# Optimization experiments

Hardware: AMD Instinct MI355X
Metric: run time of the kernel (lower is better)

Reference implementation:

```python
import jax, jax.numpy as jnp
import numpy as np

KEEP_RATIO = 0.25
BLOCK = 8
TEMP = 0.1


def setup_inputs() -> dict:
    key = jax.random.key(0)
    features = jax.random.normal(key, (8, 256, 132, 132), dtype=jnp.float32)
    return {"features": features, "enabled": 1}


def reference(features, enabled):
    B, C, H, W = features.shape
    if not enabled:
        return jnp.ones((B, C, H, W), dtype=features.dtype)
    # pad H, W up to multiples of BLOCK (zeros, like F.pad default)
    ph = (-H) % BLOCK
    pw = (-W) % BLOCK
    x = jnp.pad(jnp.abs(features), ((0, 0), (0, 0), (0, ph), (0, pw)))
    Hp, Wp = H + ph, W + pw
    nh, nw = Hp // BLOCK, Wp // BLOCK
    # avg_pool2d(kernel=stride=BLOCK) == block-mean via reshape
    pooled = x.reshape(B, C, nh, BLOCK, nw, BLOCK).mean(axis=(3, 5))  # [B,C,nh,nw]
    total = nh * nw
    scores = pooled.reshape(B, C, total)
    keep = max(1, min(total, int(round(total * KEEP_RATIO))))
    top_vals, top_idx = jax.lax.top_k(scores, keep)  # sorted descending, like torch.topk
    # hard mask: scatter ones at topk indices
    flat_idx = top_idx.reshape(B * C, keep)
    hard = (jnp.zeros((B * C, total), dtype=features.dtype)
            .at[jnp.arange(B * C)[:, None], flat_idx].set(1.0)
            .reshape(B, C, total))
    # training-mode straight-through soft blend
    thr = jax.lax.stop_gradient(top_vals[..., -1:])  # kth value as threshold
    soft = jax.nn.sigmoid((scores - thr) / TEMP)
    soft = soft * (keep / jnp.maximum(soft.sum(-1, keepdims=True), 1e-6))
    soft = jnp.clip(soft, 0.0, 1.0)
    mask = jax.lax.stop_gradient(hard) - jax.lax.stop_gradient(soft) + soft
    # upsample blocks back to pixels (repeat_interleave) and crop padding
    block_mask = mask.reshape(B, C, nh, nw)
    full = jnp.repeat(jnp.repeat(block_mask, BLOCK, axis=2), BLOCK, axis=3)
    return full[:, :, :H, :W]
```

## Files before the change

### kernel.cpp

```cpp
#include <hip/hip_runtime.h>


#define HH 132
#define WW 132
#define NB 17
#define TOTAL 289
#define NKPAD 292
#define KEEP 72
#define NTH 256
#define NC4 33
#define NV 4356
#define PLANES 2048

typedef float floatx4 __attribute__((ext_vector_type(4)));

__global__ __launch_bounds__(NTH)
void gate_kernel(const float4* __restrict__ feats4,
                 const int* __restrict__ enabled_p,
                 float4* __restrict__ out4) {
    const int plane = blockIdx.x;
    const int t = threadIdx.x;
    const float4* __restrict__ fp = feats4 + (size_t)plane * NV;

    __shared__ __align__(16) float    s_e[NV];
    __shared__ __align__(16) unsigned s_key[NKPAD];
    __shared__ float s_hard[TOTAL];

    #pragma unroll
    for (int k = 0; k < 18; ++k) {
        const int v = t + k * NTH;
        if (v < NV) {
            const float4 x = fp[v];
            s_e[v] = (fabsf(x.x) + fabsf(x.y)) + (fabsf(x.z) + fabsf(x.w));
        }
    }
    __syncthreads();

    for (int b = t; b < TOTAL; b += NTH) {
        const int br = b / NB;
        const int bc = b - br * NB;
        const int nr = (br == NB - 1) ? 4 : 8;
        const int base = (br * 8) * NC4 + 2 * bc;
        double sum = 0.0;
        if (bc < NB - 1) {
            for (int rr = 0; rr < nr; ++rr)
                sum += (double)s_e[base + rr * NC4]
                     + (double)s_e[base + rr * NC4 + 1];
        } else {
            for (int rr = 0; rr < nr; ++rr)
                sum += (double)s_e[base + rr * NC4];
        }
        s_key[b] = __float_as_uint((float)sum);
    }
    if (t < NKPAD - TOTAL) s_key[TOTAL + t] = 0u;
    __syncthreads();

    const int en = *enabled_p;
    for (int i = t; i < TOTAL; i += NTH) {
        const unsigned ki = s_key[i];
        const int thr0 = (i + 3) >> 2;
        const int thr1 = (i + 2) >> 2;
        const int thr2 = (i + 1) >> 2;
        const int thr3 =  i      >> 2;
        const uint4* __restrict__ sk4 = (const uint4*)s_key;
        int rank = 0;
        #pragma unroll 8
        for (int q = 0; q < NKPAD / 4; ++q) {
            const uint4 k = sk4[q];
            rank += (int)((k.x > ki) || ((k.x == ki) && (q < thr0)));
            rank += (int)((k.y > ki) || ((k.y == ki) && (q < thr1)));
            rank += (int)((k.z > ki) || ((k.z == ki) && (q < thr2)));
            rank += (int)((k.w > ki) || ((k.w == ki) && (q < thr3)));
        }
        s_hard[i] = (!en || rank < KEEP) ? 1.0f : 0.0f;
    }
    __syncthreads();

    floatx4* __restrict__ op = (floatx4*)(out4 + (size_t)plane * NV);
    for (int v = t; v < NV; v += NTH) {
        const int base = v * 4;
        const int row = base / WW;
        const int col = base - row * WW;
        const float m = s_hard[(row >> 3) * NB + (col >> 3)];
        const floatx4 mv = {m, m, m, m};
        __builtin_nontemporal_store(mv, &op[v]);
    }
}

extern "C" void kernel_launch(void* const* d_in, const int* in_sizes, int n_in,
                              void* d_out, int out_size, void* d_ws, size_t ws_size,
                              hipStream_t stream) {
    const float4* feats = (const float4*)d_in[0];
    const int* enabled = (const int*)d_in[1];
    float4* out = (float4*)d_out;
    gate_kernel<<<PLANES, NTH, 0, stream>>>(feats, enabled, out);
}
```

Measured before the change: 256.2 us.

## Replace O(n^2) rank counting with wavefront radix-select threshold for top-k

Instead of each thread counting how many of the 289 keys exceed its own, a single wavefront does a 32-step bitwise radix select using ballot and popcount. This finds the k-th largest key and how many of the tied keys to keep. Each element then compares against that threshold, and only exact ties scan earlier indices so the lowest-index tie-break is preserved. It removes the quadratic LDS scan but adds an extra barrier and a serial phase run by only one wavefront.

Result: no change. 260.8 us (+1.8%).

```diff
diff --git a/kernel.cpp b/kernel.cpp
--- a/kernel.cpp
+++ b/kernel.cpp
@@ -5,7 +5,7 @@
 #define WW 132
 #define NB 17
 #define TOTAL 289
-#define NKPAD 292
+#define NPAD 320
 #define KEEP 72
 #define NTH 256
 #define NC4 33
@@ -23,8 +23,10 @@
     const float4* __restrict__ fp = feats4 + (size_t)plane * NV;
 
     __shared__ __align__(16) float    s_e[NV];
-    __shared__ __align__(16) unsigned s_key[NKPAD];
+    __shared__ __align__(16) unsigned s_key[NPAD];
     __shared__ float s_hard[TOTAL];
+    __shared__ unsigned s_T;
+    __shared__ int s_kT;
 
     #pragma unroll
     for (int k = 0; k < 18; ++k) {
@@ -36,43 +38,67 @@
     }
     __syncthreads();
 
-    for (int b = t; b < TOTAL; b += NTH) {
-        const int br = b / NB;
-        const int bc = b - br * NB;
-        const int nr = (br == NB - 1) ? 4 : 8;
-        const int base = (br * 8) * NC4 + 2 * bc;
-        double sum = 0.0;
-        if (bc < NB - 1) {
-            for (int rr = 0; rr < nr; ++rr)
-                sum += (double)s_e[base + rr * NC4]
-                     + (double)s_e[base + rr * NC4 + 1];
-        } else {
-            for (int rr = 0; rr < nr; ++rr)
-                sum += (double)s_e[base + rr * NC4];
+    for (int b = t; b < NPAD; b += NTH) {
+        unsigned key = 0u;
+        if (b < TOTAL) {
+            const int br = b / NB;
+            const int bc = b - br * NB;
+            const int nr = (br == NB - 1) ? 4 : 8;
+            const int base = (br * 8) * NC4 + 2 * bc;
+            double sum = 0.0;
+            if (bc < NB - 1) {
+                for (int rr = 0; rr < nr; ++rr)
+                    sum += (double)s_e[base + rr * NC4]
+                         + (double)s_e[base + rr * NC4 + 1];
+            } else {
+                for (int rr = 0; rr < nr; ++rr)
+                    sum += (double)s_e[base + rr * NC4];
+            }
+            key = __float_as_uint((float)sum);
         }
-        s_key[b] = __float_as_uint((float)sum);
+        s_key[b] = key;
     }
-    if (t < NKPAD - TOTAL) s_key[TOTAL + t] = 0u;
+    __syncthreads();
+
+    if (t < 64) {
+        unsigned K0 = s_key[t];
+        unsigned K1 = s_key[64 + t];
+        unsigned K2 = s_key[128 + t];
+        unsigned K3 = s_key[192 + t];
+        unsigned K4 = s_key[256 + t];
+        unsigned P = 0u;
+        int k = KEEP;
+        #pragma unroll
+        for (int b = 31; b >= 0; --b) {
+            const unsigned hi = (P >> b) | 1u;
+            int cnt = __popcll(__ballot((K0 >> b) == hi))
+                    + __popcll(__ballot((K1 >> b) == hi))
+                    + __popcll(__ballot((K2 >> b) == hi))
+                    + __popcll(__ballot((K3 >> b) == hi))
+                    + __popcll(__ballot((K4 >> b) == hi));
+            if (cnt >= k) P |= (1u << b);
+            else          k -= cnt;
+        }
+        if (t == 0) { s_T = P; s_kT = k; }
+    }
     __syncthreads();
 
     const int en = *enabled_p;
+    const unsigned T = s_T;
+    const int kT = s_kT;
     for (int i = t; i < TOTAL; i += NTH) {
         const unsigned ki = s_key[i];
-        const int thr0 = (i + 3) >> 2;
-        const int thr1 = (i + 2) >> 2;
-        const int thr2 = (i + 1) >> 2;
-        const int thr3 =  i      >> 2;
-        const uint4* __restrict__ sk4 = (const uint4*)s_key;
-        int rank = 0;
-        #pragma unroll 8
-        for (int q = 0; q < NKPAD / 4; ++q) {
-            const uint4 k = sk4[q];
-            rank += (int)((k.x > ki) || ((k.x == ki) && (q < thr0)));
-            rank += (int)((k.y > ki) || ((k.y == ki) && (q < thr1)));
-            rank += (int)((k.z > ki) || ((k.z == ki) && (q < thr2)));
-            rank += (int)((k.w > ki) || ((k.w == ki) && (q < thr3)));
+        float m;
+        if (!en || ki > T) {
+            m = 1.0f;
+        } else if (ki < T) {
+            m = 0.0f;
+        } else {
+            int eq = 0;
+            for (int j = 0; j < i; ++j) eq += (int)(s_key[j] == T);
+            m = (eq < kT) ? 1.0f : 0.0f;
         }
-        s_hard[i] = (!en || rank < KEEP) ? 1.0f : 0.0f;
+        s_hard[i] = m;
     }
     __syncthreads();
 
```
